# Optimization experiments

Measured on AMD Instinct MI355X. Metric: run time of the kernel, lower is better.

Reference implementation:

```python
import jax, jax.numpy as jnp
import numpy as np

DEPTH = 2
DIM = 512
HEADS = 8
DH = 64
INNER = HEADS * DH
MLP = 2048
B = 2
N = 2048
EPS = 1e-6
NEG = -float(np.finfo(np.float32).max)
SCALE = DH ** -0.5


def setup_inputs() -> dict:
    key = jax.random.key(0)
    ks = jax.random.split(key, 8)
    inp = {
        'x': jax.random.normal(ks[0], (B, N, DIM), dtype=jnp.float32),
        'mask': jax.random.randint(ks[1], (B, N), 0, 2, dtype=jnp.int32),
        'qkv_w': 0.02 * jax.random.normal(ks[2], (DEPTH, DIM, 3 * INNER), dtype=jnp.float32),
        'out_w': 0.02 * jax.random.normal(ks[3], (DEPTH, INNER, DIM), dtype=jnp.float32),
        'out_b': jnp.zeros((DEPTH, DIM), dtype=jnp.float32),
        'ff_w1': 0.02 * jax.random.normal(ks[4], (DEPTH, DIM, MLP), dtype=jnp.float32),
        'ff_b1': jnp.zeros((DEPTH, MLP), dtype=jnp.float32),
        'ff_w2': 0.02 * jax.random.normal(ks[5], (DEPTH, MLP, DIM), dtype=jnp.float32),
        'ff_b2': jnp.zeros((DEPTH, DIM), dtype=jnp.float32),
        'ad1_w': jnp.ones((DEPTH, B * DIM), dtype=jnp.float32),
        'ad1_b': jnp.zeros((DEPTH, B * DIM), dtype=jnp.float32),
        'ad2_w': jnp.ones((DEPTH, B * DIM), dtype=jnp.float32),
        'ad2_b': jnp.zeros((DEPTH, B * DIM), dtype=jnp.float32),
    }
    return inp


def adain(x, w, b):
    # AdaptiveInstanceNorm2d: batch_norm over channels (B*D), spatial dim N, training=True
    # -> per-(b, d) mean/biased-var over N, affine params of shape (B*D,) -> (B,1,D)
    mu = jnp.mean(x, axis=1, keepdims=True)
    var = jnp.var(x, axis=1, keepdims=True)  # biased variance, as in batch_norm
    xn = (x - mu) * jax.lax.rsqrt(var + EPS)
    b_sz, _, d = x.shape
    return xn * w.reshape(b_sz, 1, d) + b.reshape(b_sz, 1, d)


def attention(x, mask2d, qkv_w, out_w, out_b):
    b_sz, n, _ = x.shape
    qkv = x @ qkv_w  # [B,N,3*INNER]
    q, k, v = jnp.split(qkv, 3, axis=-1)

    def split_heads(t):
        return t.reshape(b_sz, n, HEADS, DH).transpose(0, 2, 1, 3)  # [B,H,N,D]

    q, k, v = split_heads(q), split_heads(k), split_heads(v)
    dots = jnp.einsum('bhnd,bhmd->bhnm', q, k) * SCALE  # [B,H,N,N]
    dots = jnp.where(mask2d[:, None] == 0, NEG, dots)
    attn = jax.nn.softmax(dots, axis=-1)
    out = jnp.einsum('bhnm,bhmd->bhnd', attn, v)
    out = out.transpose(0, 2, 1, 3).reshape(b_sz, n, INNER)
    return out @ out_w + out_b


def feedforward(x, w1, b1, w2, b2):
    h = jax.nn.gelu(x @ w1 + b1, approximate=False)  # torch nn.GELU default = exact erf
    return h @ w2 + b2


def reference(x, mask, qkv_w, out_w, out_b, ff_w1, ff_b1, ff_w2, ff_b2,
              ad1_w, ad1_b, ad2_w, ad2_b):
    mask2d = mask[:, :, None] * mask[:, None, :]  # [B,N,N]
    for l in range(DEPTH):
        h = adain(x, ad1_w[l], ad1_b[l])
        x = attention(h, mask2d, qkv_w[l], out_w[l], out_b[l]) + x
        h = adain(x, ad2_w[l], ad2_b[l])
        x = feedforward(h, ff_w1[l], ff_b1[l], ff_w2[l], ff_b2[l]) + x
    return x
```

## Files before the change

### kernel.cpp

```cpp
#include <hip/hip_runtime.h>
#include <hip/hip_bf16.h>

#define DEPTHL 2
#define DIMM   512
#define NHEADS 8
#define DHH    64
#define INNERD 512
#define MLPD   2048
#define BB     2
#define SEQL   2048
#define ROWS   (BB*SEQL)
#define MNEG   (-1.0e38f)
#define SCLQ   0.18033688f
#define NSPLIT 4
#define KPS    (SEQL / NSPLIT)

typedef __attribute__((ext_vector_type(4))) float f32x4;
typedef __attribute__((ext_vector_type(8))) __bf16 bf16x8;

#define GLDS16(g, l) __builtin_amdgcn_global_load_lds((const __attribute__((address_space(1))) void*)(g), (__attribute__((address_space(3))) void*)(l), 16, 0, 0)

__device__ __forceinline__ unsigned short f2bf(float f) {
  union { float f; unsigned int u; } v; v.f = f;
  unsigned int r = v.u + 0x7fffu + ((v.u >> 16) & 1u);
  return (unsigned short)(r >> 16);
}
__device__ __forceinline__ float bf2f(unsigned short h) {
  union { unsigned int u; float f; } v; v.u = ((unsigned int)h) << 16; return v.f;
}
__device__ __forceinline__ unsigned int cvtpk(float a, float b) {
  unsigned int r;
  asm("v_cvt_pk_bf16_f32 %0, %1, %2" : "=v"(r) : "v"(a), "v"(b));
  return r;
}

__global__ __launch_bounds__(256) void wtrans(const float* __restrict__ wsrc,
                                              unsigned short* __restrict__ wdst,
                                              int K, int N) {
  __shared__ float t[32][33];
  const float* src = wsrc + (size_t)blockIdx.z * K * N;
  unsigned short* dst = wdst + (size_t)blockIdx.z * K * N;
  int k0 = blockIdx.x * 32, n0 = blockIdx.y * 32;
  int tx = threadIdx.x & 31, ty = threadIdx.x >> 5;
#pragma unroll
  for (int j = 0; j < 32; j += 8)
    t[ty + j][tx] = src[(size_t)(k0 + ty + j) * N + n0 + tx];
  __syncthreads();
#pragma unroll
  for (int j = 0; j < 32; j += 8)
    dst[(size_t)(n0 + ty + j) * K + k0 + tx] = f2bf(t[tx][ty + j]);
}

__global__ __launch_bounds__(512) void adain_p1(const float* __restrict__ x,
                                                float* __restrict__ p1, float* __restrict__ p2) {
  int d = threadIdx.x, c = blockIdx.x, b = blockIdx.y;
  const float* xp = x + ((size_t)b * SEQL + c * 64) * DIMM + d;
  float s = 0.f, s2 = 0.f;
  for (int i = 0; i < 64; ++i) { float v = xp[(size_t)i * DIMM]; s += v; s2 += v * v; }
  p1[(b * 32 + c) * DIMM + d] = s;
  p2[(b * 32 + c) * DIMM + d] = s2;
}

__global__ __launch_bounds__(512) void adain_p2(const float* __restrict__ p1, const float* __restrict__ p2,
                                                const float* __restrict__ w, const float* __restrict__ bi,
                                                float* __restrict__ alpha, float* __restrict__ beta) {
  int d = threadIdx.x, b = blockIdx.x;
  float s = 0.f, s2 = 0.f;
  for (int c = 0; c < 32; ++c) { s += p1[(b * 32 + c) * DIMM + d]; s2 += p2[(b * 32 + c) * DIMM + d]; }
  float mean = s * (1.0f / SEQL);
  float var = s2 * (1.0f / SEQL) - mean * mean;
  float a = w[b * DIMM + d] * rsqrtf(var + 1e-6f);
  alpha[b * DIMM + d] = a;
  beta[b * DIMM + d] = bi[b * DIMM + d] - mean * a;
}

__global__ __launch_bounds__(256) void adain_apply(const float* __restrict__ x,
                                                   const float* __restrict__ alpha, const float* __restrict__ beta,
                                                   unsigned short* __restrict__ hb) {
  int idx = blockIdx.x * 256 + threadIdx.x;
  int d = idx & (DIMM - 1);
  int b = idx >> 20;
  hb[idx] = f2bf(x[idx] * alpha[b * DIMM + d] + beta[b * DIMM + d]);
}

__global__ __launch_bounds__(256) void maskbuild(const int* __restrict__ mask, float* __restrict__ maskadd) {
  int i = blockIdx.x * 256 + threadIdx.x;
  maskadd[i] = mask[i] ? 0.f : MNEG;
}

template <int EPI, int BN>
__global__ __launch_bounds__(256)
void gemm_k(const unsigned short* __restrict__ A,
            const unsigned short* __restrict__ Wt,
            const float* __restrict__ bias,
            const float* __restrict__ resid,
            float* __restrict__ outF,
            unsigned short* __restrict__ outB,
            unsigned short* __restrict__ part,
            int N, int Kt) {
  constexpr int NI = BN / 32;
  __shared__ __align__(16) unsigned short As[2][128 * 32];
  __shared__ __align__(16) unsigned short Bs[2][BN * 32];
  const int tid = threadIdx.x;
  const int w = tid >> 6, lane = tid & 63;

  unsigned int f = blockIdx.y * gridDim.x + blockIdx.x;
  unsigned int grp = f & 7u, idx = f >> 3;
  unsigned int rpx = gridDim.y >> 3;
  unsigned int by = grp * rpx + idx / gridDim.x;
  unsigned int bx = idx % gridDim.x;

  const int bm = by * 128, bn = bx * BN;
  const int wm = (w >> 1) * 64, wn = (w & 1) * (BN / 2);

  const int nsplit = gridDim.z, sp = blockIdx.z;
  const int Kc = Kt / nsplit;
  const int kbeg = sp * Kc, kend = kbeg + Kc;

  f32x4 acc[4][NI] = {};

  auto stage = [&](int buf, int k0) {
#pragma unroll
    for (int j = 0; j < 2; ++j) {
      int r = w * 32 + (lane >> 2) + j * 16;
      int cl = (lane & 3) ^ ((r >> 1) & 3);
      GLDS16(A + (size_t)(bm + r) * Kt + k0 + cl * 8, &As[buf][(w * 32 + j * 16) * 32]);
    }
    if (BN == 128) {
#pragma unroll
      for (int j = 0; j < 2; ++j) {
        int r = w * 32 + (lane >> 2) + j * 16;
        int cl = (lane & 3) ^ ((r >> 1) & 3);
        GLDS16(Wt + (size_t)(bn + r) * Kt + k0 + cl * 8, &Bs[buf][(w * 32 + j * 16) * 32]);
      }
    } else {
      int r = w * 16 + (lane >> 2);
      int cl = (lane & 3) ^ ((r >> 1) & 3);
      GLDS16(Wt + (size_t)(bn + r) * Kt + k0 + cl * 8, &Bs[buf][(w * 16) * 32]);
    }
  };

  stage(0, kbeg);
  __syncthreads();
  int cur = 0;

  for (int k0 = kbeg; k0 < kend; k0 += 32) {
    if (k0 + 32 < kend) stage(cur ^ 1, k0 + 32);
    bf16x8 af[4], bfr[NI];
#pragma unroll
    for (int i = 0; i < 4; ++i) {
      int ar = wm + i * 16 + (lane & 15);
      int ac = (lane >> 4) ^ ((ar >> 1) & 3);
      af[i] = *(const bf16x8*)&As[cur][ar * 32 + ac * 8];
    }
#pragma unroll
    for (int i = 0; i < NI; ++i) {
      int br = wn + i * 16 + (lane & 15);
      int bc = (lane >> 4) ^ ((br >> 1) & 3);
      bfr[i] = *(const bf16x8*)&Bs[cur][br * 32 + bc * 8];
    }
#pragma unroll
    for (int mi = 0; mi < 4; ++mi)
#pragma unroll
      for (int ni = 0; ni < NI; ++ni)
        acc[mi][ni] = __builtin_amdgcn_mfma_f32_16x16x32_bf16(af[mi], bfr[ni], acc[mi][ni], 0, 0, 0);
    __syncthreads();
    cur ^= 1;
  }

  const size_t MN = (size_t)gridDim.y * 128 * N;
#pragma unroll
  for (int mi = 0; mi < 4; ++mi) {
#pragma unroll
    for (int ni = 0; ni < NI; ++ni) {
#pragma unroll
      for (int r = 0; r < 4; ++r) {
        int row = bm + wm + mi * 16 + (lane >> 4) * 4 + r;
        int col = bn + wn + ni * 16 + (lane & 15);
        float v = acc[mi][ni][r];
        size_t o = (size_t)row * N + col;
        if (EPI == 3) {
          part[(size_t)sp * MN + o] = f2bf(v);
        } else {
          if (bias) v += bias[col];
          if (EPI == 1) v = 0.5f * v * (1.0f + erff(v * 0.70710678118f));
          if (EPI == 2) outF[o] = v + resid[o];
          else if (EPI != 2) outB[o] = f2bf(v);
        }
      }
    }
  }
}

template <int NS>
__global__ __launch_bounds__(256) void comb_k(const unsigned short* __restrict__ part,
                                              const float* __restrict__ bias,
                                              const float* __restrict__ resid,
                                              float* __restrict__ outF) {
  size_t idx = ((size_t)blockIdx.x * 256 + threadIdx.x) * 4;
  int col = (int)(idx & 511);
  float a0 = 0.f, a1 = 0.f, a2 = 0.f, a3 = 0.f;
#pragma unroll
  for (int s = 0; s < NS; ++s) {
    uint2 v = *(const uint2*)&part[(size_t)s * ROWS * 512 + idx];
    a0 += bf2f(v.x & 0xffff); a1 += bf2f(v.x >> 16);
    a2 += bf2f(v.y & 0xffff); a3 += bf2f(v.y >> 16);
  }
  f32x4 b = *(const f32x4*)&bias[col];
  f32x4 rs = *(const f32x4*)&resid[idx];
  f32x4 o;
  o[0] = a0 + b[0] + rs[0]; o[1] = a1 + b[1] + rs[1];
  o[2] = a2 + b[2] + rs[2]; o[3] = a3 + b[3] + rs[3];
  *(f32x4*)&outF[idx] = o;
}

__global__ __launch_bounds__(256) void qkv_prep(const unsigned short* __restrict__ qkv,
                                                unsigned short* __restrict__ q,
                                                unsigned short* __restrict__ k,
                                                unsigned short* __restrict__ vt,
                                                float* __restrict__ vsum) {
  __shared__ unsigned short t[64][65];
  const int bh = blockIdx.x, nt = blockIdx.y;
  const int b = bh >> 3, h = bh & 7;
  const int n0 = nt * 64;
  const int tid = threadIdx.x;
  const int nloc = tid >> 3, dh0 = (tid & 7) * 8;
#pragma unroll
  for (int j = 0; j < 2; ++j) {
    int n = nloc + j * 32;
    size_t src = (size_t)(b * SEQL + n0 + n) * 1536 + h * 64 + dh0;
    size_t dst = ((size_t)bh * SEQL + n0 + n) * 64 + dh0;
    uint4 qv = *(const uint4*)&qkv[src];
    uint4 qs;
    qs.x = cvtpk(bf2f(qv.x & 0xffff) * SCLQ, bf2f(qv.x >> 16) * SCLQ);
    qs.y = cvtpk(bf2f(qv.y & 0xffff) * SCLQ, bf2f(qv.y >> 16) * SCLQ);
    qs.z = cvtpk(bf2f(qv.z & 0xffff) * SCLQ, bf2f(qv.z >> 16) * SCLQ);
    qs.w = cvtpk(bf2f(qv.w & 0xffff) * SCLQ, bf2f(qv.w >> 16) * SCLQ);
    *(uint4*)&q[dst] = qs;
    *(uint4*)&k[dst] = *(const uint4*)&qkv[src + INNERD];
    uint4 vv = *(const uint4*)&qkv[src + 2 * INNERD];
    unsigned short* tr = &t[n][dh0];
    tr[0] = (unsigned short)(vv.x & 0xffff); tr[1] = (unsigned short)(vv.x >> 16);
    tr[2] = (unsigned short)(vv.y & 0xffff); tr[3] = (unsigned short)(vv.y >> 16);
    tr[4] = (unsigned short)(vv.z & 0xffff); tr[5] = (unsigned short)(vv.z >> 16);
    tr[6] = (unsigned short)(vv.w & 0xffff); tr[7] = (unsigned short)(vv.w >> 16);
  }
  __syncthreads();
#pragma unroll
  for (int j = 0; j < 16; ++j) {
    int i = tid + j * 256;
    int dh = i >> 6, n = i & 63;
    vt[((size_t)bh * DHH + dh) * SEQL + n0 + n] = t[n][dh];
  }
  int dh = tid >> 2, seg = tid & 3;
  float s = 0.f;
#pragma unroll
  for (int i = 0; i < 16; ++i) s += bf2f(t[seg * 16 + i][dh]);
  s += __shfl_xor(s, 1);
  s += __shfl_xor(s, 2);
  if (seg == 0) atomicAdd(&vsum[bh * 64 + dh], s);
}

__global__ __launch_bounds__(256, 4)
void attn_split(const unsigned short* __restrict__ qg,
                const unsigned short* __restrict__ kg,
                const unsigned short* __restrict__ vtg,
                const float* __restrict__ maskadd,
                unsigned short* __restrict__ opart,
                float* __restrict__ lpart) {
  __shared__ __align__(16) unsigned short Ks[64 * 64];
  __shared__ __align__(16) unsigned short Vts[64 * 64];
  __shared__ __align__(16) unsigned short Ps[4 * 32 * 64];
  const int tid = threadIdx.x, w = tid >> 6, lane = tid & 63;
  const int g = lane >> 4, c = lane & 15;
  const int bh = blockIdx.y, b = bh >> 3;
  const int qt = blockIdx.x;
  const int split = blockIdx.z;
  const int kv0 = split * KPS;
  const int q0 = qt * 128 + w * 32;
  const float* maskb = maskadd + b * SEQL;

  bf16x8 qf0[2], qf1[2];
#pragma unroll
  for (int kb = 0; kb < 2; ++kb) {
    qf0[kb] = *(const bf16x8*)&qg[((size_t)bh * SEQL + q0 + c) * DHH + kb * 32 + g * 8];
    qf1[kb] = *(const bf16x8*)&qg[((size_t)bh * SEQL + q0 + 16 + c) * DHH + kb * 32 + g * 8];
  }

  const __bf16 one1 = (__bf16)1.0f;
  const bf16x8 ones = {one1, one1, one1, one1, one1, one1, one1, one1};

  f32x4 o0[4] = {}, o1[4] = {};
  f32x4 lones0 = {}, lones1 = {};
  unsigned short* myP = &Ps[w * 2048];

  for (int kt = 0; kt < KPS / 64; ++kt) {
#pragma unroll
    for (int j = 0; j < 2; ++j) {
      int r = w * 16 + j * 8 + (lane >> 3);
      int cl = (lane & 7) ^ (r & 7);
      GLDS16(kg + ((size_t)bh * SEQL + kv0 + kt * 64 + r) * DHH + cl * 8, &Ks[(w * 16 + j * 8) * 64]);
      GLDS16(vtg + ((size_t)bh * DHH + r) * SEQL + kv0 + kt * 64 + cl * 8, &Vts[(w * 16 + j * 8) * 64]);
    }
    __syncthreads();

    f32x4 sT0[4], sT1[4];
#pragma unroll
    for (int nt = 0; nt < 4; ++nt) {
      f32x4 mk = *(const f32x4*)&maskb[kv0 + kt * 64 + nt * 16 + g * 4];
      sT0[nt] = mk;
      sT1[nt] = mk;
    }
#pragma unroll
    for (int nt = 0; nt < 4; ++nt) {
#pragma unroll
      for (int kb = 0; kb < 2; ++kb) {
        int kr = nt * 16 + c;
        int cs = (kb * 4 + g) ^ (kr & 7);
        bf16x8 kf = *(const bf16x8*)&Ks[kr * 64 + cs * 8];
        sT0[nt] = __builtin_amdgcn_mfma_f32_16x16x32_bf16(kf, qf0[kb], sT0[nt], 0, 0, 0);
        sT1[nt] = __builtin_amdgcn_mfma_f32_16x16x32_bf16(kf, qf1[kb], sT1[nt], 0, 0, 0);
      }
    }

#pragma unroll
    for (int nt = 0; nt < 4; ++nt) {
      int swz = (((nt * 2 + (g >> 1)) ^ (c & 7)) << 3) + ((g & 1) << 2);
      {
        float pv0 = exp2f(sT0[nt][0]), pv1 = exp2f(sT0[nt][1]);
        float pv2 = exp2f(sT0[nt][2]), pv3 = exp2f(sT0[nt][3]);
        *(uint2*)(myP + c * 64 + swz) = make_uint2(cvtpk(pv0, pv1), cvtpk(pv2, pv3));
      }
      {
        float pv0 = exp2f(sT1[nt][0]), pv1 = exp2f(sT1[nt][1]);
        float pv2 = exp2f(sT1[nt][2]), pv3 = exp2f(sT1[nt][3]);
        *(uint2*)(myP + (16 + c) * 64 + swz) = make_uint2(cvtpk(pv0, pv1), cvtpk(pv2, pv3));
      }
    }

#pragma unroll
    for (int kb = 0; kb < 2; ++kb) {
      int ps = ((kb * 4 + g) ^ (c & 7)) << 3;
      bf16x8 pf0 = *(const bf16x8*)&myP[c * 64 + ps];
      bf16x8 pf1 = *(const bf16x8*)&myP[(16 + c) * 64 + ps];
      lones0 = __builtin_amdgcn_mfma_f32_16x16x32_bf16(pf0, ones, lones0, 0, 0, 0);
      lones1 = __builtin_amdgcn_mfma_f32_16x16x32_bf16(pf1, ones, lones1, 0, 0, 0);
#pragma unroll
      for (int ni = 0; ni < 4; ++ni) {
        int vr = ni * 16 + c;
        int vc = (kb * 4 + g) ^ (vr & 7);
        bf16x8 vf = *(const bf16x8*)&Vts[vr * 64 + vc * 8];
        o0[ni] = __builtin_amdgcn_mfma_f32_16x16x32_bf16(pf0, vf, o0[ni], 0, 0, 0);
        o1[ni] = __builtin_amdgcn_mfma_f32_16x16x32_bf16(pf1, vf, o1[ni], 0, 0, 0);
      }
    }
    __syncthreads();
  }

  const size_t pb = ((size_t)split * 16 + bh) * SEQL;
#pragma unroll
  for (int ni = 0; ni < 4; ++ni) {
#pragma unroll
    for (int r = 0; r < 4; ++r) {
      opart[(pb + q0 + g * 4 + r) * DHH + ni * 16 + c] = f2bf(o0[ni][r]);
      opart[(pb + q0 + 16 + g * 4 + r) * DHH + ni * 16 + c] = f2bf(o1[ni][r]);
    }
  }
  if (c == 0) {
#pragma unroll
    for (int r = 0; r < 4; ++r) {
      lpart[pb + q0 + g * 4 + r] = lones0[r];
      lpart[pb + q0 + 16 + g * 4 + r] = lones1[r];
    }
  }
}

__global__ __launch_bounds__(256) void attn_combine(const unsigned short* __restrict__ opart,
                                                    const float* __restrict__ lpart,
                                                    const float* __restrict__ maskadd,
                                                    const float* __restrict__ vsum,
                                                    unsigned short* __restrict__ ctx) {
  int idx = blockIdx.x * 256 + threadIdx.x;
  int dq = idx & 15;
  int q = (idx >> 4) & (SEQL - 1);
  int bh = idx >> 15;
  int d0 = dq * 4;
  int b = bh >> 3, h = bh & 7;
  float o0 = 0.f, o1 = 0.f, o2 = 0.f, o3 = 0.f, L = 0.f;
#pragma unroll
  for (int s = 0; s < NSPLIT; ++s) {
    size_t base = ((size_t)s * 16 + bh) * SEQL + q;
    L += lpart[base];
    uint2 v = *(const uint2*)&opart[base * DHH + d0];
    o0 += bf2f(v.x & 0xffff); o1 += bf2f(v.x >> 16);
    o2 += bf2f(v.y & 0xffff); o3 += bf2f(v.y >> 16);
  }
  float r = 1.0f / L;
  o0 *= r; o1 *= r; o2 *= r; o3 *= r;
  if (maskadd[b * SEQL + q] != 0.f) {
    f32x4 vm = *(const f32x4*)&vsum[bh * 64 + d0];
    o0 = vm[0] * (1.0f / SEQL); o1 = vm[1] * (1.0f / SEQL);
    o2 = vm[2] * (1.0f / SEQL); o3 = vm[3] * (1.0f / SEQL);
  }
  *(uint2*)&ctx[((size_t)(b * SEQL + q)) * INNERD + h * 64 + d0] =
      make_uint2(cvtpk(o0, o1), cvtpk(o2, o3));
}

extern "C" void kernel_launch(void* const* d_in, const int* in_sizes, int n_in,
                              void* d_out, int out_size, void* d_ws, size_t ws_size,
                              hipStream_t stream) {
  (void)in_sizes; (void)n_in; (void)out_size;
  const float* x_in = (const float*)d_in[0];
  const int* mask = (const int*)d_in[1];
  const float* qkv_w = (const float*)d_in[2];
  const float* out_w = (const float*)d_in[3];
  const float* out_b = (const float*)d_in[4];
  const float* ff_w1 = (const float*)d_in[5];
  const float* ff_b1 = (const float*)d_in[6];
  const float* ff_w2 = (const float*)d_in[7];
  const float* ff_b2 = (const float*)d_in[8];
  const float* ad1w = (const float*)d_in[9];
  const float* ad1b = (const float*)d_in[10];
  const float* ad2w = (const float*)d_in[11];
  const float* ad2b = (const float*)d_in[12];

  char* ws = (char*)d_ws;
  size_t off = 0;
  auto alloc = [&](size_t bytes) {
    char* p = ws + off;
    off = (off + bytes + 255) & ~(size_t)255;
    return p;
  };
  unsigned short* wtQ = (unsigned short*)alloc((size_t)DEPTHL * 1536 * 512 * 2);
  unsigned short* wtO = (unsigned short*)alloc((size_t)DEPTHL * 512 * 512 * 2);
  unsigned short* wtF1 = (unsigned short*)alloc((size_t)DEPTHL * 2048 * 512 * 2);
  unsigned short* wtF2 = (unsigned short*)alloc((size_t)DEPTHL * 512 * 2048 * 2);
  float* xc = (float*)alloc((size_t)ROWS * DIMM * 4);
  unsigned short* hbf = (unsigned short*)alloc((size_t)ROWS * DIMM * 2);
  unsigned short* qkvbf = (unsigned short*)alloc((size_t)ROWS * 1536 * 2);
  char* region2 = alloc((size_t)4 * 16 * SEQL * DHH * 2);
  unsigned short* qb = (unsigned short*)region2;
  unsigned short* kb = qb + (size_t)16 * SEQL * DHH;
  unsigned short* vtb = kb + (size_t)16 * SEQL * DHH;
  unsigned short* ctxb = vtb + (size_t)16 * SEQL * DHH;
  unsigned short* h1bf = (unsigned short*)region2;
  float* p1 = (float*)alloc((size_t)BB * 32 * DIMM * 4);
  float* p2 = (float*)alloc((size_t)BB * 32 * DIMM * 4);
  float* alpha = (float*)alloc((size_t)BB * DIMM * 4);
  float* beta = (float*)alloc((size_t)BB * DIMM * 4);
  float* maskadd = (float*)alloc((size_t)BB * SEQL * 4);
  unsigned short* opart = (unsigned short*)alloc((size_t)NSPLIT * 16 * SEQL * DHH * 2);
  float* lpart = (float*)alloc((size_t)NSPLIT * 16 * SEQL * 4);
  float* vsum = (float*)alloc((size_t)16 * 64 * 4);
  unsigned short* part = (unsigned short*)alloc((size_t)4 * ROWS * 512 * 2);
  const bool fits = off <= ws_size;

  hipMemcpyAsync(xc, x_in, (size_t)ROWS * DIMM * 4, hipMemcpyDeviceToDevice, stream);

  wtrans<<<dim3(512 / 32, 1536 / 32, DEPTHL), 256, 0, stream>>>(qkv_w, wtQ, 512, 1536);
  wtrans<<<dim3(512 / 32, 512 / 32, DEPTHL), 256, 0, stream>>>(out_w, wtO, 512, 512);
  wtrans<<<dim3(512 / 32, 2048 / 32, DEPTHL), 256, 0, stream>>>(ff_w1, wtF1, 512, 2048);
  wtrans<<<dim3(2048 / 32, 512 / 32, DEPTHL), 256, 0, stream>>>(ff_w2, wtF2, 2048, 512);
  maskbuild<<<BB * SEQL / 256, 256, 0, stream>>>(mask, maskadd);

  for (int l = 0; l < DEPTHL; ++l) {
    adain_p1<<<dim3(32, BB), 512, 0, stream>>>(xc, p1, p2);
    adain_p2<<<BB, 512, 0, stream>>>(p1, p2, ad1w + l * BB * DIMM, ad1b + l * BB * DIMM, alpha, beta);
    adain_apply<<<8192, 256, 0, stream>>>(xc, alpha, beta, hbf);
    gemm_k<0, 64><<<dim3(1536 / 64, ROWS / 128), 256, 0, stream>>>(
        hbf, wtQ + (size_t)l * 1536 * 512, nullptr, nullptr, nullptr, qkvbf, nullptr, 1536, 512);
    hipMemsetAsync(vsum, 0, 16 * 64 * 4, stream);
    qkv_prep<<<dim3(16, 32), 256, 0, stream>>>(qkvbf, qb, kb, vtb, vsum);
    attn_split<<<dim3(SEQL / 128, 16, NSPLIT), 256, 0, stream>>>(qb, kb, vtb, maskadd, opart, lpart);
    attn_combine<<<16 * SEQL * 16 / 256, 256, 0, stream>>>(opart, lpart, maskadd, vsum, ctxb);
    if (fits) {
      gemm_k<3, 64><<<dim3(512 / 64, ROWS / 128, 2), 256, 0, stream>>>(
          ctxb, wtO + (size_t)l * 512 * 512, nullptr, nullptr, nullptr, nullptr, part, 512, 512);
      comb_k<2><<<ROWS * 512 / 1024, 256, 0, stream>>>(part, out_b + l * DIMM, xc, xc);
    } else {
      gemm_k<2, 64><<<dim3(512 / 64, ROWS / 128), 256, 0, stream>>>(
          ctxb, wtO + (size_t)l * 512 * 512, out_b + l * DIMM, xc, xc, nullptr, nullptr, 512, 512);
    }
    adain_p1<<<dim3(32, BB), 512, 0, stream>>>(xc, p1, p2);
    adain_p2<<<BB, 512, 0, stream>>>(p1, p2, ad2w + l * BB * DIMM, ad2b + l * BB * DIMM, alpha, beta);
    adain_apply<<<8192, 256, 0, stream>>>(xc, alpha, beta, hbf);
    gemm_k<1, 64><<<dim3(2048 / 64, ROWS / 128), 256, 0, stream>>>(
        hbf, wtF1 + (size_t)l * 2048 * 512, ff_b1 + l * MLPD, nullptr, nullptr, h1bf, nullptr, 2048, 512);
    float* xout = (l == DEPTHL - 1) ? (float*)d_out : xc;
    if (fits) {
      gemm_k<3, 64><<<dim3(512 / 64, ROWS / 128, 4), 256, 0, stream>>>(
          h1bf, wtF2 + (size_t)l * 512 * 2048, nullptr, nullptr, nullptr, nullptr, part, 512, 2048);
      comb_k<4><<<ROWS * 512 / 1024, 256, 0, stream>>>(part, ff_b2 + l * DIMM, xc, xout);
    } else {
      gemm_k<2, 64><<<dim3(512 / 64, ROWS / 128), 256, 0, stream>>>(
          h1bf, wtF2 + (size_t)l * 512 * 2048, ff_b2 + l * DIMM, xc, xout, nullptr, nullptr, 512, 2048);
    }
  }
}
```

Measured before the change: 312.6 us.

## Fuse QKV head split into GEMM epilogue and widen AdaIN reductions

Result: faster. 285.0 us (-8.8%).

```diff
diff --git a/kernel.cpp b/kernel.cpp
--- a/kernel.cpp
+++ b/kernel.cpp
@@ -14,6 +14,7 @@
 #define SCLQ   0.18033688f
 #define NSPLIT 4
 #define KPS    (SEQL / NSPLIT)
+#define NCH    128
 
 typedef __attribute__((ext_vector_type(4))) float f32x4;
 typedef __attribute__((ext_vector_type(8))) __bf16 bf16x8;
@@ -54,33 +55,52 @@
 __global__ __launch_bounds__(512) void adain_p1(const float* __restrict__ x,
                                                 float* __restrict__ p1, float* __restrict__ p2) {
   int d = threadIdx.x, c = blockIdx.x, b = blockIdx.y;
-  const float* xp = x + ((size_t)b * SEQL + c * 64) * DIMM + d;
+  const float* xp = x + ((size_t)b * SEQL + c * 16) * DIMM + d;
   float s = 0.f, s2 = 0.f;
-  for (int i = 0; i < 64; ++i) { float v = xp[(size_t)i * DIMM]; s += v; s2 += v * v; }
-  p1[(b * 32 + c) * DIMM + d] = s;
-  p2[(b * 32 + c) * DIMM + d] = s2;
+#pragma unroll
+  for (int i = 0; i < 16; ++i) { float v = xp[(size_t)i * DIMM]; s += v; s2 += v * v; }
+  p1[(b * NCH + c) * DIMM + d] = s;
+  p2[(b * NCH + c) * DIMM + d] = s2;
 }
 
 __global__ __launch_bounds__(512) void adain_p2(const float* __restrict__ p1, const float* __restrict__ p2,
                                                 const float* __restrict__ w, const float* __restrict__ bi,
                                                 float* __restrict__ alpha, float* __restrict__ beta) {
-  int d = threadIdx.x, b = blockIdx.x;
+  __shared__ float redA[8][64], redB[8][64];
+  int b = blockIdx.x, dg = blockIdx.y;
+  int dl = threadIdx.x & 63, seg = threadIdx.x >> 6;
+  int d = dg * 64 + dl;
   float s = 0.f, s2 = 0.f;
-  for (int c = 0; c < 32; ++c) { s += p1[(b * 32 + c) * DIMM + d]; s2 += p2[(b * 32 + c) * DIMM + d]; }
-  float mean = s * (1.0f / SEQL);
-  float var = s2 * (1.0f / SEQL) - mean * mean;
-  float a = w[b * DIMM + d] * rsqrtf(var + 1e-6f);
-  alpha[b * DIMM + d] = a;
-  beta[b * DIMM + d] = bi[b * DIMM + d] - mean * a;
+#pragma unroll
+  for (int i = 0; i < 16; ++i) {
+    int c = seg * 16 + i;
+    s += p1[(b * NCH + c) * DIMM + d];
+    s2 += p2[(b * NCH + c) * DIMM + d];
+  }
+  redA[seg][dl] = s; redB[seg][dl] = s2;
+  __syncthreads();
+  if (seg == 0) {
+#pragma unroll
+    for (int i = 1; i < 8; ++i) { s += redA[i][dl]; s2 += redB[i][dl]; }
+    float mean = s * (1.0f / SEQL);
+    float var = s2 * (1.0f / SEQL) - mean * mean;
+    float a = w[b * DIMM + d] * rsqrtf(var + 1e-6f);
+    alpha[b * DIMM + d] = a;
+    beta[b * DIMM + d] = bi[b * DIMM + d] - mean * a;
+  }
 }
 
 __global__ __launch_bounds__(256) void adain_apply(const float* __restrict__ x,
                                                    const float* __restrict__ alpha, const float* __restrict__ beta,
                                                    unsigned short* __restrict__ hb) {
-  int idx = blockIdx.x * 256 + threadIdx.x;
+  int idx = (blockIdx.x * 256 + threadIdx.x) * 4;
   int d = idx & (DIMM - 1);
   int b = idx >> 20;
-  hb[idx] = f2bf(x[idx] * alpha[b * DIMM + d] + beta[b * DIMM + d]);
+  f32x4 xv = *(const f32x4*)&x[idx];
+  f32x4 av = *(const f32x4*)&alpha[b * DIMM + d];
+  f32x4 bv = *(const f32x4*)&beta[b * DIMM + d];
+  *(uint2*)&hb[idx] = make_uint2(cvtpk(xv[0] * av[0] + bv[0], xv[1] * av[1] + bv[1]),
+                                 cvtpk(xv[2] * av[2] + bv[2], xv[3] * av[3] + bv[3]));
 }
 
 __global__ __launch_bounds__(256) void maskbuild(const int* __restrict__ mask, float* __restrict__ maskadd) {
@@ -97,6 +117,9 @@
             float* __restrict__ outF,
             unsigned short* __restrict__ outB,
             unsigned short* __restrict__ part,
+            unsigned short* __restrict__ qg4,
+            unsigned short* __restrict__ kg4,
+            unsigned short* __restrict__ vt4,
             int N, int Kt) {
   constexpr int NI = BN / 32;
   __shared__ __align__(16) unsigned short As[2][128 * 32];
@@ -178,14 +201,23 @@
         int row = bm + wm + mi * 16 + (lane >> 4) * 4 + r;
         int col = bn + wn + ni * 16 + (lane & 15);
         float v = acc[mi][ni][r];
-        size_t o = (size_t)row * N + col;
-        if (EPI == 3) {
-          part[(size_t)sp * MN + o] = f2bf(v);
+        if (EPI == 4) {
+          int brow = row >> 11, n = row & (SEQL - 1);
+          int sec = col >> 9, h = (col >> 6) & 7, dh = col & 63;
+          int bh = brow * 8 + h;
+          if (sec == 0) qg4[((size_t)bh * SEQL + n) * DHH + dh] = f2bf(v * SCLQ);
+          else if (sec == 1) kg4[((size_t)bh * SEQL + n) * DHH + dh] = f2bf(v);
+          else vt4[((size_t)bh * DHH + dh) * SEQL + n] = f2bf(v);
         } else {
-          if (bias) v += bias[col];
-          if (EPI == 1) v = 0.5f * v * (1.0f + erff(v * 0.70710678118f));
-          if (EPI == 2) outF[o] = v + resid[o];
-          else if (EPI != 2) outB[o] = f2bf(v);
+          size_t o = (size_t)row * N + col;
+          if (EPI == 3) {
+            part[(size_t)sp * MN + o] = f2bf(v);
+          } else {
+            if (bias) v += bias[col];
+            if (EPI == 1) v = 0.5f * v * (1.0f + erff(v * 0.70710678118f));
+            if (EPI == 2) outF[o] = v + resid[o];
+            else outB[o] = f2bf(v);
+          }
         }
       }
     }
@@ -214,51 +246,26 @@
   *(f32x4*)&outF[idx] = o;
 }
 
-__global__ __launch_bounds__(256) void qkv_prep(const unsigned short* __restrict__ qkv,
-                                                unsigned short* __restrict__ q,
-                                                unsigned short* __restrict__ k,
-                                                unsigned short* __restrict__ vt,
-                                                float* __restrict__ vsum) {
-  __shared__ unsigned short t[64][65];
-  const int bh = blockIdx.x, nt = blockIdx.y;
-  const int b = bh >> 3, h = bh & 7;
-  const int n0 = nt * 64;
-  const int tid = threadIdx.x;
-  const int nloc = tid >> 3, dh0 = (tid & 7) * 8;
-#pragma unroll
-  for (int j = 0; j < 2; ++j) {
-    int n = nloc + j * 32;
-    size_t src = (size_t)(b * SEQL + n0 + n) * 1536 + h * 64 + dh0;
-    size_t dst = ((size_t)bh * SEQL + n0 + n) * 64 + dh0;
-    uint4 qv = *(const uint4*)&qkv[src];
-    uint4 qs;
-    qs.x = cvtpk(bf2f(qv.x & 0xffff) * SCLQ, bf2f(qv.x >> 16) * SCLQ);
-    qs.y = cvtpk(bf2f(qv.y & 0xffff) * SCLQ, bf2f(qv.y >> 16) * SCLQ);
-    qs.z = cvtpk(bf2f(qv.z & 0xffff) * SCLQ, bf2f(qv.z >> 16) * SCLQ);
-    qs.w = cvtpk(bf2f(qv.w & 0xffff) * SCLQ, bf2f(qv.w >> 16) * SCLQ);
-    *(uint4*)&q[dst] = qs;
-    *(uint4*)&k[dst] = *(const uint4*)&qkv[src + INNERD];
-    uint4 vv = *(const uint4*)&qkv[src + 2 * INNERD];
-    unsigned short* tr = &t[n][dh0];
-    tr[0] = (unsigned short)(vv.x & 0xffff); tr[1] = (unsigned short)(vv.x >> 16);
-    tr[2] = (unsigned short)(vv.y & 0xffff); tr[3] = (unsigned short)(vv.y >> 16);
-    tr[4] = (unsigned short)(vv.z & 0xffff); tr[5] = (unsigned short)(vv.z >> 16);
-    tr[6] = (unsigned short)(vv.w & 0xffff); tr[7] = (unsigned short)(vv.w >> 16);
-  }
+__global__ __launch_bounds__(256) void vmean_k(const unsigned short* __restrict__ vt,
+                                               float* __restrict__ vmean) {
+  __shared__ float red[256];
+  int bh = blockIdx.x, t = threadIdx.x;
+  int d = blockIdx.y * 8 + (t >> 5), seg = t & 31;
+  const unsigned short* p = vt + ((size_t)bh * 64 + d) * SEQL + seg * 64;
+  float s = 0.f;
+#pragma unroll
+  for (int i = 0; i < 16; ++i) {
+    uint2 v = *(const uint2*)&p[i * 4];
+    s += bf2f(v.x & 0xffff) + bf2f(v.x >> 16) + bf2f(v.y & 0xffff) + bf2f(v.y >> 16);
+  }
+  red[t] = s;
   __syncthreads();
-#pragma unroll
-  for (int j = 0; j < 16; ++j) {
-    int i = tid + j * 256;
-    int dh = i >> 6, n = i & 63;
-    vt[((size_t)bh * DHH + dh) * SEQL + n0 + n] = t[n][dh];
-  }
-  int dh = tid >> 2, seg = tid & 3;
-  float s = 0.f;
-#pragma unroll
-  for (int i = 0; i < 16; ++i) s += bf2f(t[seg * 16 + i][dh]);
-  s += __shfl_xor(s, 1);
-  s += __shfl_xor(s, 2);
-  if (seg == 0) atomicAdd(&vsum[bh * 64 + dh], s);
+  if (t < 8) {
+    float a = 0.f;
+#pragma unroll
+    for (int i = 0; i < 32; ++i) a += red[t * 32 + i];
+    vmean[bh * 64 + blockIdx.y * 8 + t] = a * (1.0f / SEQL);
+  }
 }
 
 __global__ __launch_bounds__(256, 4)
@@ -378,7 +385,7 @@
 __global__ __launch_bounds__(256) void attn_combine(const unsigned short* __restrict__ opart,
                                                     const float* __restrict__ lpart,
                                                     const float* __restrict__ maskadd,
-                                                    const float* __restrict__ vsum,
+                                                    const float* __restrict__ vmean,
                                                     unsigned short* __restrict__ ctx) {
   int idx = blockIdx.x * 256 + threadIdx.x;
   int dq = idx & 15;
@@ -398,9 +405,8 @@
   float r = 1.0f / L;
   o0 *= r; o1 *= r; o2 *= r; o3 *= r;
   if (maskadd[b * SEQL + q] != 0.f) {
-    f32x4 vm = *(const f32x4*)&vsum[bh * 64 + d0];
-    o0 = vm[0] * (1.0f / SEQL); o1 = vm[1] * (1.0f / SEQL);
-    o2 = vm[2] * (1.0f / SEQL); o3 = vm[3] * (1.0f / SEQL);
+    f32x4 vm = *(const f32x4*)&vmean[bh * 64 + d0];
+    o0 = vm[0]; o1 = vm[1]; o2 = vm[2]; o3 = vm[3];
   }
   *(uint2*)&ctx[((size_t)(b * SEQL + q)) * INNERD + h * 64 + d0] =
       make_uint2(cvtpk(o0, o1), cvtpk(o2, o3));
@@ -437,25 +443,22 @@
   unsigned short* wtF2 = (unsigned short*)alloc((size_t)DEPTHL * 512 * 2048 * 2);
   float* xc = (float*)alloc((size_t)ROWS * DIMM * 4);
   unsigned short* hbf = (unsigned short*)alloc((size_t)ROWS * DIMM * 2);
-  unsigned short* qkvbf = (unsigned short*)alloc((size_t)ROWS * 1536 * 2);
   char* region2 = alloc((size_t)4 * 16 * SEQL * DHH * 2);
   unsigned short* qb = (unsigned short*)region2;
   unsigned short* kb = qb + (size_t)16 * SEQL * DHH;
   unsigned short* vtb = kb + (size_t)16 * SEQL * DHH;
   unsigned short* ctxb = vtb + (size_t)16 * SEQL * DHH;
   unsigned short* h1bf = (unsigned short*)region2;
-  float* p1 = (float*)alloc((size_t)BB * 32 * DIMM * 4);
-  float* p2 = (float*)alloc((size_t)BB * 32 * DIMM * 4);
+  float* p1 = (float*)alloc((size_t)BB * NCH * DIMM * 4);
+  float* p2 = (float*)alloc((size_t)BB * NCH * DIMM * 4);
   float* alpha = (float*)alloc((size_t)BB * DIMM * 4);
   float* beta = (float*)alloc((size_t)BB * DIMM * 4);
   float* maskadd = (float*)alloc((size_t)BB * SEQL * 4);
   unsigned short* opart = (unsigned short*)alloc((size_t)NSPLIT * 16 * SEQL * DHH * 2);
   float* lpart = (float*)alloc((size_t)NSPLIT * 16 * SEQL * 4);
-  float* vsum = (float*)alloc((size_t)16 * 64 * 4);
+  float* vmean = (float*)alloc((size_t)16 * 64 * 4);
   unsigned short* part = (unsigned short*)alloc((size_t)4 * ROWS * 512 * 2);
   const bool fits = off <= ws_size;
-
-  hipMemcpyAsync(xc, x_in, (size_t)ROWS * DIMM * 4, hipMemcpyDeviceToDevice, stream);
 
   wtrans<<<dim3(512 / 32, 1536 / 32, DEPTHL), 256, 0, stream>>>(qkv_w, wtQ, 512, 1536);
   wtrans<<<dim3(512 / 32, 512 / 32, DEPTHL), 256, 0, stream>>>(out_w, wtO, 512, 512);
@@ -464,36 +467,42 @@
   maskbuild<<<BB * SEQL / 256, 256, 0, stream>>>(mask, maskadd);
 
   for (int l = 0; l < DEPTHL; ++l) {
-    adain_p1<<<dim3(32, BB), 512, 0, stream>>>(xc, p1, p2);
-    adain_p2<<<BB, 512, 0, stream>>>(p1, p2, ad1w + l * BB * DIMM, ad1b + l * BB * DIMM, alpha, beta);
-    adain_apply<<<8192, 256, 0, stream>>>(xc, alpha, beta, hbf);
-    gemm_k<0, 64><<<dim3(1536 / 64, ROWS / 128), 256, 0, stream>>>(
-        hbf, wtQ + (size_t)l * 1536 * 512, nullptr, nullptr, nullptr, qkvbf, nullptr, 1536, 512);
-    hipMemsetAsync(vsum, 0, 16 * 64 * 4, stream);
-    qkv_prep<<<dim3(16, 32), 256, 0, stream>>>(qkvbf, qb, kb, vtb, vsum);
+    const float* xr = (l == 0) ? x_in : xc;
+    adain_p1<<<dim3(NCH, BB), 512, 0, stream>>>(xr, p1, p2);
+    adain_p2<<<dim3(BB, 8), 512, 0, stream>>>(p1, p2, ad1w + l * BB * DIMM, ad1b + l * BB * DIMM, alpha, beta);
+    adain_apply<<<2048, 256, 0, stream>>>(xr, alpha, beta, hbf);
+    gemm_k<4, 64><<<dim3(1536 / 64, ROWS / 128), 256, 0, stream>>>(
+        hbf, wtQ + (size_t)l * 1536 * 512, nullptr, nullptr, nullptr, nullptr, nullptr,
+        qb, kb, vtb, 1536, 512);
+    vmean_k<<<dim3(16, 8), 256, 0, stream>>>(vtb, vmean);
     attn_split<<<dim3(SEQL / 128, 16, NSPLIT), 256, 0, stream>>>(qb, kb, vtb, maskadd, opart, lpart);
-    attn_combine<<<16 * SEQL * 16 / 256, 256, 0, stream>>>(opart, lpart, maskadd, vsum, ctxb);
+    attn_combine<<<16 * SEQL * 16 / 256, 256, 0, stream>>>(opart, lpart, maskadd, vmean, ctxb);
     if (fits) {
       gemm_k<3, 64><<<dim3(512 / 64, ROWS / 128, 2), 256, 0, stream>>>(
-          ctxb, wtO + (size_t)l * 512 * 512, nullptr, nullptr, nullptr, nullptr, part, 512, 512);
-      comb_k<2><<<ROWS * 512 / 1024, 256, 0, stream>>>(part, out_b + l * DIMM, xc, xc);
+          ctxb, wtO + (size_t)l * 512 * 512, nullptr, nullptr, nullptr, nullptr, part,
+          nullptr, nullptr, nullptr, 512, 512);
+      comb_k<2><<<ROWS * 512 / 1024, 256, 0, stream>>>(part, out_b + l * DIMM, xr, xc);
     } else {
       gemm_k<2, 64><<<dim3(512 / 64, ROWS / 128), 256, 0, stream>>>(
-          ctxb, wtO + (size_t)l * 512 * 512, out_b + l * DIMM, xc, xc, nullptr, nullptr, 512, 512);
-    }
-    adain_p1<<<dim3(32, BB), 512, 0, stream>>>(xc, p1, p2);
-    adain_p2<<<BB, 512, 0, stream>>>(p1, p2, ad2w + l * BB * DIMM, ad2b + l * BB * DIMM, alpha, beta);
-    adain_apply<<<8192, 256, 0, stream>>>(xc, alpha, beta, hbf);
+          ctxb, wtO + (size_t)l * 512 * 512, out_b + l * DIMM, xr, xc, nullptr, nullptr,
+          nullptr, nullptr, nullptr, 512, 512);
+    }
+    adain_p1<<<dim3(NCH, BB), 512, 0, stream>>>(xc, p1, p2);
+    adain_p2<<<dim3(BB, 8), 512, 0, stream>>>(p1, p2, ad2w + l * BB * DIMM, ad2b + l * BB * DIMM, alpha, beta);
+    adain_apply<<<2048, 256, 0, stream>>>(xc, alpha, beta, hbf);
     gemm_k<1, 64><<<dim3(2048 / 64, ROWS / 128), 256, 0, stream>>>(
-        hbf, wtF1 + (size_t)l * 2048 * 512, ff_b1 + l * MLPD, nullptr, nullptr, h1bf, nullptr, 2048, 512);
+        hbf, wtF1 + (size_t)l * 2048 * 512, ff_b1 + l * MLPD, nullptr, nullptr, h1bf, nullptr,
+        nullptr, nullptr, nullptr, 2048, 512);
     float* xout = (l == DEPTHL - 1) ? (float*)d_out : xc;
     if (fits) {
       gemm_k<3, 64><<<dim3(512 / 64, ROWS / 128, 4), 256, 0, stream>>>(
-          h1bf, wtF2 + (size_t)l * 512 * 2048, nullptr, nullptr, nullptr, nullptr, part, 512, 2048);
+          h1bf, wtF2 + (size_t)l * 512 * 2048, nullptr, nullptr, nullptr, nullptr, part,
+          nullptr, nullptr, nullptr, 512, 2048);
       comb_k<4><<<ROWS * 512 / 1024, 256, 0, stream>>>(part, ff_b2 + l * DIMM, xc, xout);
     } else {
       gemm_k<2, 64><<<dim3(512 / 64, ROWS / 128), 256, 0, stream>>>(
-          h1bf, wtF2 + (size_t)l * 512 * 2048, ff_b2 + l * DIMM, xc, xout, nullptr, nullptr, 512, 2048);
-    }
-  }
-}
+          h1bf, wtF2 + (size_t)l * 512 * 2048, ff_b2 + l * DIMM, xc, xout, nullptr, nullptr,
+          nullptr, nullptr, nullptr, 512, 2048);
+    }
+  }
+}
```
